# Performance work log

Hardware: AMD Instinct MI355X
Metric: run time of the kernel (lower is better)

The kernel has to match this reference:

```python
import jax, jax.numpy as jnp
import numpy as np


def setup_inputs() -> dict:
    key = jax.random.key(0)
    k1, k2 = jax.random.split(key)
    n, h, L, d = 4, 16, 1024, 64
    max_positions = 512
    query = jax.random.normal(k1, (n, h, L, d), dtype=jnp.float32)
    rel_emb = jax.random.normal(k2, (h, d, 2 * max_positions + 1), dtype=jnp.float32)
    return {"query": query, "rel_emb": rel_emb, "length": L}


def reference(query, rel_emb, length):
    # logits: [n, h, i, 2*max_positions+1]
    logits = jnp.einsum('nhid,hdj->nhij', query, rel_emb)
    max_positions = (rel_emb.shape[-1] - 1) // 2
    idx = jnp.arange(length)
    # relative offsets grid [i, j] = j - i  (last=False path)
    grid = idx[None, :] - idx[:, None]
    # clamp to valid range and shift to table indices
    table_idx = jnp.clip(grid, 1 - max_positions, max_positions - 1) + max_positions
    n, h = logits.shape[0], logits.shape[1]
    gather_idx = jnp.broadcast_to(table_idx[None, None, :, :], (n, h, length, length))
    # out[n,h,i,j] = logits[n,h,i,table_idx[i,j]]
    out = jnp.take_along_axis(logits, gather_idx, axis=-1)
    return out
```

## Files before the change

kernel.cpp:

```cpp
#include <hip/hip_runtime.h>
#include <hip/hip_bf16.h>


#define NH 16
#define LQ 1024
#define DD 64
#define TT 1025
#define MAXP 512
#define PADS 4
#define LSTRIDE2 1036
#define UNITS 8

typedef float f32x4 __attribute__((ext_vector_type(4)));
typedef short s16x4 __attribute__((ext_vector_type(4)));
typedef short s16x8 __attribute__((ext_vector_type(8)));

__device__ __forceinline__ short f2bf(float f) {
    __hip_bfloat16 h = __float2bfloat16(f);
    return __builtin_bit_cast(short, h);
}
__device__ __forceinline__ float bf2f(short s) {
    return __builtin_bit_cast(float, ((unsigned)(unsigned short)s) << 16);
}

template<int D>
__device__ __forceinline__ void write_chunks(const unsigned short* __restrict__ lrow,
                                             float p1, float p2,
                                             int i, int l, float* __restrict__ orow) {
    #pragma unroll
    for (int c = 0; c < 4; ++c) {
        const int j0 = c * 256 + 4 * l;
        const int t0 = j0 - i + MAXP;
        int colA = PADS + t0 - D;
        colA = colA < 0 ? 0 : (colA > PADS + LQ ? PADS + LQ : colA);
        s16x4 A = *(const s16x4*)(lrow + colA);
        s16x4 B = {0, 0, 0, 0};
        if (D) B = *(const s16x4*)(lrow + colA + 4);
        f32x4 v;
        #pragma unroll
        for (int e = 0; e < 4; ++e) {
            const int t = t0 + e;
            const float in = bf2f((D + e < 4) ? A[D + e] : B[D + e - 4]);
            v[e] = t < 1 ? p1 : (t > LQ - 1 ? p2 : in);
        }
        __builtin_nontemporal_store(v, (f32x4*)(orow + j0));
    }
}

__global__ __launch_bounds__(256, 2) void lpb_pc(const float* __restrict__ Q,
                                                 const float* __restrict__ R,
                                                 float* __restrict__ out) {
    __shared__ unsigned short lg[2][16][LSTRIDE2];

    const int bidx = blockIdx.x;
    const int swz  = (bidx & 7) * 64 + (bidx >> 3);
    const int nh   = swz >> 3;
    const int ibg  = swz & 7;
    const int h    = nh & (NH - 1);

    const int tid = threadIdx.x;
    const int w = tid >> 6, l = tid & 63;
    const int n = l & 15, g = l >> 4;

    const float* rbase = R + (size_t)(h * DD + 8 * g) * TT;

    #pragma unroll 1
    for (int rnd = 0; rnd <= UNITS; ++rnd) {
        if (w < 2) {
            if (rnd < UNITS) {
                const int ibase = (ibg * UNITS + rnd) * 16;
                const float* qrow = Q + ((size_t)nh * LQ + (ibase + n)) * DD + 8 * g;
                s16x8 qf[2];
                #pragma unroll
                for (int kh = 0; kh < 2; ++kh) {
                    f32x4 a = *(const f32x4*)(qrow + kh * 32);
                    f32x4 b = *(const f32x4*)(qrow + kh * 32 + 4);
                    #pragma unroll
                    for (int e = 0; e < 4; ++e) { qf[kh][e] = f2bf(a[e]); qf[kh][4 + e] = f2bf(b[e]); }
                }
                unsigned short (*buf)[LSTRIDE2] = lg[rnd & 1];
                #pragma unroll 4
                for (int mt = 0; mt < 32; ++mt) {
                    const int tb = w * 512 + mt * 16;
                    const float* rc = rbase + tb + n;
                    s16x8 rf0, rf1;
                    #pragma unroll
                    for (int e = 0; e < 8; ++e) {
                        rf0[e] = f2bf(rc[(size_t)e * TT]);
                        rf1[e] = f2bf(rc[(size_t)(32 + e) * TT]);
                    }
                    f32x4 acc = (f32x4){0.f, 0.f, 0.f, 0.f};
                    acc = __builtin_amdgcn_mfma_f32_16x16x32_bf16(rf0, qf[0], acc, 0, 0, 0);
                    acc = __builtin_amdgcn_mfma_f32_16x16x32_bf16(rf1, qf[1], acc, 0, 0, 0);
                    s16x4 hv;
                    #pragma unroll
                    for (int s = 0; s < 4; ++s) hv[s] = f2bf(acc[s]);
                    *(s16x4*)&buf[n][PADS + tb + 4 * g] = hv;
                }
            }
        } else {
            if (rnd > 0) {
                const int u = rnd - 1;
                const int ibase = (ibg * UNITS + u) * 16;
                unsigned short (*buf)[LSTRIDE2] = lg[u & 1];
                const int cw = w - 2;
                #pragma unroll 1
                for (int rr = 0; rr < 8; ++rr) {
                    const int il = cw * 8 + rr;
                    const int i  = ibase + il;
                    const unsigned short* lrow = &buf[il][0];
                    const float p1 = bf2f(lrow[PADS + 1]);
                    const float p2 = bf2f(lrow[PADS + LQ - 1]);
                    float* orow = out + ((size_t)nh * LQ + i) * LQ;
                    switch ((MAXP - i) & 3) {
                        case 0: write_chunks<0>(lrow, p1, p2, i, l, orow); break;
                        case 1: write_chunks<1>(lrow, p1, p2, i, l, orow); break;
                        case 2: write_chunks<2>(lrow, p1, p2, i, l, orow); break;
                        default: write_chunks<3>(lrow, p1, p2, i, l, orow); break;
                    }
                }
            }
        }
        __syncthreads();
    }
}

extern "C" void kernel_launch(void* const* d_in, const int* in_sizes, int n_in,
                              void* d_out, int out_size, void* d_ws, size_t ws_size,
                              hipStream_t stream) {
    const float* Q = (const float*)d_in[0];
    const float* R = (const float*)d_in[1];
    float* out = (float*)d_out;

    lpb_pc<<<dim3(512), 256, 0, stream>>>(Q, R, out);
}
```

Measured before the change: 74.19 us.

## Pretranspose rel_emb to bf16 workspace and widen blocks to 512 threads

Measured after the change: 99.31 us. 33.9% more time.

```diff
diff --git a/kernel.cpp b/kernel.cpp
--- a/kernel.cpp
+++ b/kernel.cpp
@@ -23,6 +23,19 @@
     return __builtin_bit_cast(float, ((unsigned)(unsigned short)s) << 16);
 }
 
+__global__ __launch_bounds__(256) void lpb_pret(const float* __restrict__ R,
+                                                short* __restrict__ Rt) {
+    const int t = blockIdx.x * 256 + threadIdx.x;
+    if (t >= TT) return;
+    const int hk = blockIdx.y;
+    const int h = hk >> 3, kb = hk & 7;
+    const float* rp = R + (size_t)(h * DD + kb * 8) * TT + t;
+    s16x8 v;
+    #pragma unroll
+    for (int r = 0; r < 8; ++r) v[r] = f2bf(rp[(size_t)r * TT]);
+    *(s16x8*)(Rt + (size_t)(h * TT + t) * DD + kb * 8) = v;
+}
+
 template<int D>
 __device__ __forceinline__ void write_chunks(const unsigned short* __restrict__ lrow,
                                              float p1, float p2,
@@ -43,12 +56,14 @@
             const float in = bf2f((D + e < 4) ? A[D + e] : B[D + e - 4]);
             v[e] = t < 1 ? p1 : (t > LQ - 1 ? p2 : in);
         }
-        __builtin_nontemporal_store(v, (f32x4*)(orow + j0));
+        *(f32x4*)(orow + j0) = v;
     }
 }
 
-__global__ __launch_bounds__(256, 2) void lpb_pc(const float* __restrict__ Q,
+template<bool PRET>
+__global__ __launch_bounds__(512, 4) void lpb_pc(const float* __restrict__ Q,
                                                  const float* __restrict__ R,
+                                                 const short* __restrict__ Rt,
                                                  float* __restrict__ out) {
     __shared__ unsigned short lg[2][16][LSTRIDE2];
 
@@ -61,8 +76,6 @@
     const int tid = threadIdx.x;
     const int w = tid >> 6, l = tid & 63;
     const int n = l & 15, g = l >> 4;
-
-    const float* rbase = R + (size_t)(h * DD + 8 * g) * TT;
 
     #pragma unroll 1
     for (int rnd = 0; rnd <= UNITS; ++rnd) {
@@ -82,12 +95,18 @@
                 #pragma unroll 4
                 for (int mt = 0; mt < 32; ++mt) {
                     const int tb = w * 512 + mt * 16;
-                    const float* rc = rbase + tb + n;
                     s16x8 rf0, rf1;
-                    #pragma unroll
-                    for (int e = 0; e < 8; ++e) {
-                        rf0[e] = f2bf(rc[(size_t)e * TT]);
-                        rf1[e] = f2bf(rc[(size_t)(32 + e) * TT]);
+                    if (PRET) {
+                        const short* rp = Rt + ((size_t)h * TT + tb + n) * DD + 8 * g;
+                        rf0 = *(const s16x8*)rp;
+                        rf1 = *(const s16x8*)(rp + 32);
+                    } else {
+                        const float* rc = R + (size_t)(h * DD + 8 * g) * TT + tb + n;
+                        #pragma unroll
+                        for (int e = 0; e < 8; ++e) {
+                            rf0[e] = f2bf(rc[(size_t)e * TT]);
+                            rf1[e] = f2bf(rc[(size_t)(32 + e) * TT]);
+                        }
                     }
                     f32x4 acc = (f32x4){0.f, 0.f, 0.f, 0.f};
                     acc = __builtin_amdgcn_mfma_f32_16x16x32_bf16(rf0, qf[0], acc, 0, 0, 0);
@@ -105,10 +124,9 @@
                 unsigned short (*buf)[LSTRIDE2] = lg[u & 1];
                 const int cw = w - 2;
                 #pragma unroll 1
-                for (int rr = 0; rr < 8; ++rr) {
-                    const int il = cw * 8 + rr;
-                    const int i  = ibase + il;
-                    const unsigned short* lrow = &buf[il][0];
+                for (int rr = cw; rr < 16; rr += 6) {
+                    const int i  = ibase + rr;
+                    const unsigned short* lrow = &buf[rr][0];
                     const float p1 = bf2f(lrow[PADS + 1]);
                     const float p2 = bf2f(lrow[PADS + LQ - 1]);
                     float* orow = out + ((size_t)nh * LQ + i) * LQ;
@@ -132,5 +150,12 @@
     const float* R = (const float*)d_in[1];
     float* out = (float*)d_out;
 
-    lpb_pc<<<dim3(512), 256, 0, stream>>>(Q, R, out);
+    const size_t RT_BYTES = (size_t)NH * TT * DD * sizeof(short);
+    if (ws_size >= RT_BYTES) {
+        short* Rt = (short*)d_ws;
+        lpb_pret<<<dim3(5, NH * 8), 256, 0, stream>>>(R, Rt);
+        lpb_pc<true><<<dim3(512), 512, 0, stream>>>(Q, R, Rt, out);
+    } else {
+        lpb_pc<false><<<dim3(512), 512, 0, stream>>>(Q, R, nullptr, out);
+    }
 }
```
